# Optimization experiments

Hardware: AMD Instinct MI355X
Metric: run time of the kernel (lower is better)

## Reference

```python
import jax, jax.numpy as jnp
import numpy as np

N = 50000      # nodes
E = 800000     # edges (avg degree 16)
D = 128        # feature / channel width (channel_counts=[128,128,128])
HEAD = 64      # head_dim
NEG_SLOPE = 0.2  # PyG GATConv leaky_relu slope


def setup_inputs() -> dict:
    key = jax.random.key(0)
    ks = jax.random.split(key, 32)
    s = 1.0 / np.sqrt(D)

    def w(k, shape):
        return jax.random.normal(k, shape, jnp.float32) * s

    return {
        "x": jax.random.normal(ks[0], (N, D), jnp.float32),
        "edge_index": jax.random.randint(ks[1], (2, E), 0, N, dtype=jnp.int32),
        # layer 0: lazy (-1,-1) GATConv -> separate src/dst linear maps
        "w0_src": w(ks[2], (D, D)), "w0_dst": w(ks[3], (D, D)),
        "a0_src": w(ks[4], (D,)), "a0_dst": w(ks[5], (D,)),
        "bc0": jnp.zeros((D,), jnp.float32),
        "wl0": w(ks[6], (D, D)), "bl0": jnp.zeros((D,), jnp.float32),
        # layer 1: int in_channels -> shared weight
        "w1": w(ks[7], (D, D)),
        "a1_src": w(ks[8], (D,)), "a1_dst": w(ks[9], (D,)),
        "bc1": jnp.zeros((D,), jnp.float32),
        "wl1": w(ks[10], (D, D)), "bl1": jnp.zeros((D,), jnp.float32),
        # layer 2
        "w2": w(ks[11], (D, D)),
        "a2_src": w(ks[12], (D,)), "a2_dst": w(ks[13], (D,)),
        "bc2": jnp.zeros((D,), jnp.float32),
        "wl2": w(ks[14], (D, D)), "bl2": jnp.zeros((D,), jnp.float32),
        # head linear
        "wh": w(ks[15], (D, HEAD)), "bh": jnp.zeros((HEAD,), jnp.float32),
    }


def _gat(h_src, h_dst, src, dst, a_src, a_dst, bias):
    """PyG GATConv (heads=1, no self loops, eval-mode). h_*: [N,C]."""
    al_s = h_src @ a_src                                   # [N]
    al_d = h_dst @ a_dst                                   # [N]
    logits = jax.nn.leaky_relu(al_s[src] + al_d[dst], NEG_SLOPE)  # [E]
    m = jax.ops.segment_max(logits, dst, num_segments=N)  # per-dest max
    e = jnp.exp(logits - m[dst])
    denom = jax.ops.segment_sum(e, dst, num_segments=N)
    alpha = e / denom[dst]                                 # [E]
    msg = h_src[src] * alpha[:, None]                      # [E,C]
    return jax.ops.segment_sum(msg, dst, num_segments=N) + bias


def reference(x, edge_index, w0_src, w0_dst, a0_src, a0_dst, bc0, wl0, bl0,
              w1, a1_src, a1_dst, bc1, wl1, bl1,
              w2, a2_src, a2_dst, bc2, wl2, bl2, wh, bh):
    src, dst = edge_index[0], edge_index[1]
    # layer 0: conv(x) + lin(x), relu
    h = _gat(x @ w0_src, x @ w0_dst, src, dst, a0_src, a0_dst, bc0) + x @ wl0 + bl0
    h = jax.nn.relu(h)
    # layer 1: shared-weight conv
    hs = h @ w1
    h = _gat(hs, hs, src, dst, a1_src, a1_dst, bc1) + h @ wl1 + bl1
    h = jax.nn.relu(h)
    # layer 2 (no relu)
    hs = h @ w2
    h = _gat(hs, hs, src, dst, a2_src, a2_dst, bc2) + h @ wl2 + bl2
    # head
    return h @ wh + bh
```

## Files before the change

kernel.cpp:

```cpp
#include <hip/hip_runtime.h>

#define NNODE 50000
#define NEDGE 800000
#define DIM   128
#define NEG   0.2f
#define NBUCK 196
#define EPB1  2048
#define NB1   391
#define GBLK  782
#define GN    12500
#define SB_PA (NB1)
#define SB_PH (SB_PA + 32)
#define SB_MV (SB_PH + 9)
#define SB_CV (SB_MV + 193)
#define SB_TOT (SB_CV + GN)

typedef __attribute__((ext_vector_type(8))) short bf16x8;
typedef __attribute__((ext_vector_type(4))) float f32x4;

__device__ __forceinline__ float wmax(float v){
  #pragma unroll
  for (int m = 32; m > 0; m >>= 1) v = fmaxf(v, __shfl_xor(v, m));
  return v;
}
__device__ __forceinline__ float wsum(float v){
  #pragma unroll
  for (int m = 32; m > 0; m >>= 1) v += __shfl_xor(v, m);
  return v;
}
__device__ __forceinline__ unsigned short f2bf(float f){
  unsigned int x = __float_as_uint(f);
  return (unsigned short)((x + 0x7fffu + ((x >> 16) & 1u)) >> 16);
}
__device__ __forceinline__ float bflo(unsigned u){ return __uint_as_float(u << 16); }
__device__ __forceinline__ float bfhi(unsigned u){ return __uint_as_float(u & 0xffff0000u); }

__global__ __launch_bounds__(256) void setup_k(
    const int* __restrict__ ei,
    const float* __restrict__ x,
    const float* __restrict__ w0s, const float* __restrict__ a0s,
    const float* __restrict__ w0d, const float* __restrict__ a0d,
    const float* __restrict__ bc0, const float* __restrict__ wl0,
    const float* __restrict__ bl0,
    const float* __restrict__ w1,  const float* __restrict__ a1s,
    const float* __restrict__ a1d, const float* __restrict__ bc1,
    const float* __restrict__ wl1, const float* __restrict__ bl1,
    const float* __restrict__ w2,  const float* __restrict__ a2s,
    const float* __restrict__ a2d, const float* __restrict__ bc2,
    const float* __restrict__ wl2, const float* __restrict__ bl2,
    const float* __restrict__ wh,  const float* __restrict__ bh,
    int* __restrict__ cnt,
    unsigned short* __restrict__ Wz1, unsigned short* __restrict__ Wz2,
    unsigned short* __restrict__ Wz3, float* __restrict__ bf3,
    float* __restrict__ uv, float* __restrict__ bf1, float* __restrict__ bf2,
    unsigned int* __restrict__ Xb, float* __restrict__ als, float* __restrict__ ald){
  int bid = blockIdx.x;

  if (bid < NB1){
    __shared__ int h[NBUCK];
    const int* dst = ei + NEDGE;
    for (int i = threadIdx.x; i < NBUCK; i += 256) h[i] = 0;
    __syncthreads();
    int e0 = bid * EPB1 + threadIdx.x;
    #pragma unroll
    for (int i = 0; i < 8; ++i){
      int e = e0 + i * 256;
      if (e < NEDGE) atomicAdd(&h[dst[e] >> 8], 1);
    }
    __syncthreads();
    for (int i = threadIdx.x; i < NBUCK; i += 256)
      cnt[i * NB1 + bid] = h[i];
    return;
  }
  if (bid < SB_PH){
    int g = (bid - SB_PA) * 256 + threadIdx.x;
    int layer = g >> 12;
    int rem = g & 4095;
    int ct = rem >> 9, q = (rem >> 6) & 7, lane = rem & 63;
    int quad = lane >> 4;
    int c = ct * 16 + (lane & 15);
    const float* wA = layer ? w1 : w0s;
    const float* wB = layer ? wl1 : wl0;
    unsigned short* dst = (layer ? Wz2 : Wz1) + ((size_t)(ct * 8 + q) * 64 + lane) * 8;
    #pragma unroll
    for (int j = 0; j < 8; ++j){
      int k = q * 32 + quad * 8 + j;
      float v = (k < 128) ? wA[k * 128 + c] : wB[(k - 128) * 128 + c];
      dst[j] = f2bf(v);
    }
    return;
  }
  if (bid < SB_MV){
    int pb = bid - SB_PH;
    if (pb == 8){
      int c = threadIdx.x;
      if (c < 64){
        float s = bh[c];
        for (int t = 0; t < 128; ++t) s += (bc2[t] + bl2[t]) * wh[t * 64 + c];
        bf3[c] = s;
      }
      return;
    }
    int g = pb * 256 + threadIdx.x;
    int ct = g >> 9, q = (g >> 6) & 7, lane = g & 63;
    int quad = lane >> 4;
    int c = ct * 16 + (lane & 15);
    unsigned short* dst = Wz3 + ((size_t)(ct * 8 + q) * 64 + lane) * 8;
    #pragma unroll
    for (int j = 0; j < 8; ++j){
      int k = q * 32 + quad * 8 + j;
      const float* src = (k < 128) ? (w2 + k * 128) : (wl2 + (k - 128) * 128);
      float s = 0.f;
      for (int t = 0; t < 128; ++t) s += src[t] * wh[t * 64 + c];
      dst[j] = f2bf(s);
    }
    return;
  }
  if (bid < SB_CV){
    int mb = bid - SB_MV;
    if (mb == 192){
      int t = threadIdx.x;
      if (t < 128) bf1[t] = bc0[t] + bl0[t];
      else bf2[t - 128] = bc1[t - 128] + bl1[t - 128];
      return;
    }
    int lane = threadIdx.x & 63;
    int idx = mb * 4 + (threadIdx.x >> 6);
    int grp = idx >> 7, r = idx & 127;
    const float* W; const float* a;
    switch (grp){
      case 0: W = w0s; a = a0s; break;
      case 1: W = w0d; a = a0d; break;
      case 2: W = w1;  a = a1s; break;
      case 3: W = w1;  a = a1d; break;
      case 4: W = w2;  a = a2s; break;
      default: W = w2; a = a2d; break;
    }
    float2 w = ((const float2*)(W + r * DIM))[lane];
    float2 av = ((const float2*)a)[lane];
    float s = wsum(w.x * av.x + w.y * av.y);
    if (lane == 0) uv[grp * 128 + r] = s;
    return;
  }
  {
    int lane = threadIdx.x & 63;
    int n = (bid - SB_CV) * 4 + (threadIdx.x >> 6);
    if (n >= NNODE) return;
    float2 xv = ((const float2*)(x + (size_t)n * DIM))[lane];
    Xb[(size_t)n * 64 + lane] = (unsigned)f2bf(xv.x) | ((unsigned)f2bf(xv.y) << 16);
    float2 uu = ((const float2*)uv)[lane];
    float2 vv = ((const float2*)(uv + 128))[lane];
    float s1 = wsum(xv.x * uu.x + xv.y * uu.y);
    float s2 = wsum(xv.x * vv.x + xv.y * vv.y);
    if (lane == 0){ als[n] = s1; ald[n] = s2; }
  }
}


__global__ __launch_bounds__(256) void dual_k(const float* __restrict__ X,
                                              const float* __restrict__ uv,
                                              float* __restrict__ als,
                                              float* __restrict__ ald){
  int lane = threadIdx.x & 63;
  int n = blockIdx.x * 4 + (threadIdx.x >> 6);
  if (n >= NNODE) return;
  float2 xv = ((const float2*)(X + (size_t)n * DIM))[lane];
  float2 uu = ((const float2*)uv)[lane];
  float2 vv = ((const float2*)(uv + 128))[lane];
  float s1 = wsum(xv.x * uu.x + xv.y * uu.y);
  float s2 = wsum(xv.x * vv.x + xv.y * vv.y);
  if (lane == 0){ als[n] = s1; ald[n] = s2; }
}

__global__ __launch_bounds__(256) void scan196_k(const int* __restrict__ cnt,
                                                 int* __restrict__ cbase,
                                                 int* __restrict__ btot){
  __shared__ int sd[256];
  int b = blockIdx.x, t = threadIdx.x;
  const int* row = cnt + (size_t)b * NB1;
  int i0 = t * 2, i1 = t * 2 + 1;
  int v0 = (i0 < NB1) ? row[i0] : 0;
  int v1 = (i1 < NB1) ? row[i1] : 0;
  int s = v0 + v1;
  sd[t] = s; __syncthreads();
  #pragma unroll
  for (int off = 1; off < 256; off <<= 1){
    int u = (t >= off) ? sd[t - off] : 0;
    __syncthreads();
    sd[t] += u;
    __syncthreads();
  }
  int ex = sd[t] - s;
  if (i0 < NB1) cbase[(size_t)b * NB1 + i0] = ex;
  if (i1 < NB1) cbase[(size_t)b * NB1 + i1] = ex + v0;
  if (t == 255) btot[b] = sd[255];
}

__global__ __launch_bounds__(256) void bscan2_k(const int* __restrict__ btot,
                                                int* __restrict__ gbase,
                                                int* __restrict__ rp){
  __shared__ int sd[256];
  int t = threadIdx.x;
  int v = (t < NBUCK) ? btot[t] : 0;
  sd[t] = v; __syncthreads();
  #pragma unroll
  for (int off = 1; off < 256; off <<= 1){
    int u = (t >= off) ? sd[t - off] : 0;
    __syncthreads();
    sd[t] += u;
    __syncthreads();
  }
  if (t < NBUCK) gbase[t] = sd[t] - v;
  if (t == NBUCK - 1) gbase[NBUCK] = sd[t];
  if (t == 0) rp[NNODE] = NEDGE;
}

__global__ __launch_bounds__(256) void scat2_k(const int* __restrict__ ei,
                                               const int* __restrict__ gbase,
                                               const int* __restrict__ cbase,
                                               unsigned int* __restrict__ packed){
  __shared__ int lcur[NBUCK];
  for (int i = threadIdx.x; i < NBUCK; i += 256) lcur[i] = 0;
  __syncthreads();
  int e0 = blockIdx.x * EPB1 + threadIdx.x;
  #pragma unroll
  for (int i = 0; i < 8; ++i){
    int e = e0 + i * 256;
    if (e < NEDGE){
      int s = ei[e], d = ei[NEDGE + e];
      int b = d >> 8;
      int r = atomicAdd(&lcur[b], 1);
      int pos = gbase[b] + cbase[(size_t)b * NB1 + blockIdx.x] + r;
      packed[pos] = ((unsigned)d << 16) | (unsigned)s;
    }
  }
}

__global__ __launch_bounds__(256) void build_k(const int* __restrict__ gbase,
                                               const unsigned int* __restrict__ packed,
                                               int* __restrict__ rp,
                                               unsigned short* __restrict__ es){
  __shared__ int h[256], sd[256], cur[256];
  int b = blockIdx.x, t = threadIdx.x;
  int s0 = gbase[b], s1 = gbase[b + 1];
  h[t] = 0; __syncthreads();
  for (int i = s0 + t; i < s1; i += 256)
    atomicAdd(&h[(packed[i] >> 16) & 255], 1);
  __syncthreads();
  int v = h[t]; sd[t] = v; __syncthreads();
  #pragma unroll
  for (int off = 1; off < 256; off <<= 1){
    int u = (t >= off) ? sd[t - off] : 0;
    __syncthreads();
    sd[t] += u;
    __syncthreads();
  }
  int ex = sd[t] - v;
  cur[t] = ex;
  int d = b * 256 + t;
  if (d < NNODE) rp[d] = s0 + ex;
  __syncthreads();
  for (int i = s0 + t; i < s1; i += 256){
    unsigned int p = packed[i];
    int ld = (p >> 16) & 255;
    int pos = atomicAdd(&cur[ld], 1);
    es[s0 + pos] = (unsigned short)(p & 0xffffu);
  }
}

__global__ __launch_bounds__(256) void gat_k(const int* __restrict__ rp,
                                             const unsigned short* __restrict__ es,
                                             const float* __restrict__ als,
                                             const float* __restrict__ ald,
                                             const unsigned int* __restrict__ A,
                                             unsigned int* __restrict__ Mb){
  int lane = threadIdx.x & 63;
  int n = blockIdx.x * 4 + (threadIdx.x >> 6);
  if (n >= NNODE) return;
  int start = rp[n], end = rp[n + 1];
  int deg = end - start;
  float ad = ald[n];
  float2 acc = make_float2(0.f, 0.f);
  float rinv = 0.f;

  if (deg <= 64){
    int s = 0; float z = -3.0e38f;
    if (lane < deg){
      s = es[start + lane];
      float t = als[s] + ad;
      z = t > 0.f ? t : NEG * t;
    }
    float m = wmax(z);
    float e = (lane < deg) ? __expf(z - m) : 0.f;
    float denom = wsum(e);
    rinv = (deg > 0) ? 1.f / denom : 0.f;
    int dq = (deg + 7) & ~7;
    for (int j = 0; j < dq; j += 8){
      int   s0 = __shfl(s, j),     s1 = __shfl(s, j + 1);
      int   s2 = __shfl(s, j + 2), s3 = __shfl(s, j + 3);
      int   s4 = __shfl(s, j + 4), s5 = __shfl(s, j + 5);
      int   s6 = __shfl(s, j + 6), s7 = __shfl(s, j + 7);
      float w0 = __shfl(e, j),     w1 = __shfl(e, j + 1);
      float w2 = __shfl(e, j + 2), w3 = __shfl(e, j + 3);
      float w4 = __shfl(e, j + 4), w5 = __shfl(e, j + 5);
      float w6 = __shfl(e, j + 6), w7 = __shfl(e, j + 7);
      unsigned p0 = A[(size_t)s0 * 64 + lane];
      unsigned p1 = A[(size_t)s1 * 64 + lane];
      unsigned p2 = A[(size_t)s2 * 64 + lane];
      unsigned p3 = A[(size_t)s3 * 64 + lane];
      unsigned p4 = A[(size_t)s4 * 64 + lane];
      unsigned p5 = A[(size_t)s5 * 64 + lane];
      unsigned p6 = A[(size_t)s6 * 64 + lane];
      unsigned p7 = A[(size_t)s7 * 64 + lane];
      acc.x = fmaf(w0, bflo(p0), acc.x); acc.y = fmaf(w0, bfhi(p0), acc.y);
      acc.x = fmaf(w1, bflo(p1), acc.x); acc.y = fmaf(w1, bfhi(p1), acc.y);
      acc.x = fmaf(w2, bflo(p2), acc.x); acc.y = fmaf(w2, bfhi(p2), acc.y);
      acc.x = fmaf(w3, bflo(p3), acc.x); acc.y = fmaf(w3, bfhi(p3), acc.y);
      acc.x = fmaf(w4, bflo(p4), acc.x); acc.y = fmaf(w4, bfhi(p4), acc.y);
      acc.x = fmaf(w5, bflo(p5), acc.x); acc.y = fmaf(w5, bfhi(p5), acc.y);
      acc.x = fmaf(w6, bflo(p6), acc.x); acc.y = fmaf(w6, bfhi(p6), acc.y);
      acc.x = fmaf(w7, bflo(p7), acc.x); acc.y = fmaf(w7, bfhi(p7), acc.y);
    }
  } else {
    float mloc = -3.0e38f;
    for (int i = start + lane; i < end; i += 64){
      int s = es[i];
      float zz = als[s] + ad;
      zz = zz > 0.f ? zz : NEG * zz;
      mloc = fmaxf(mloc, zz);
    }
    float m = wmax(mloc);
    float dloc = 0.f;
    for (int i = start + lane; i < end; i += 64){
      int s = es[i];
      float zz = als[s] + ad;
      zz = zz > 0.f ? zz : NEG * zz;
      dloc += __expf(zz - m);
    }
    rinv = 1.f / wsum(dloc);
    for (int i = start; i < end; ++i){
      int s = es[i];
      float zz = als[s] + ad;
      zz = zz > 0.f ? zz : NEG * zz;
      float w = __expf(zz - m);
      unsigned p = A[(size_t)s * 64 + lane];
      acc.x = fmaf(w, bflo(p), acc.x);
      acc.y = fmaf(w, bfhi(p), acc.y);
    }
  }

  Mb[(size_t)n * 64 + lane] =
      (unsigned)f2bf(acc.x * rinv) | ((unsigned)f2bf(acc.y * rinv) << 16);
}

template<int FINAL>
__global__ __launch_bounds__(256) void mfma_k(const unsigned int* __restrict__ Mb,
                                              const unsigned int* __restrict__ Hin,
                                              const unsigned short* __restrict__ Wz,
                                              const float* __restrict__ bias,
                                              const float* __restrict__ u,
                                              const float* __restrict__ v,
                                              unsigned short* __restrict__ Hout,
                                              float* __restrict__ outf,
                                              float* __restrict__ als,
                                              float* __restrict__ ald){
  int lane = threadIdx.x & 63;
  int wid  = threadIdx.x >> 6;
  int r0   = blockIdx.x * 64 + wid * 16;
  int quad = lane >> 4;
  int col  = lane & 15;

  int rA = r0 + col; if (rA > NNODE - 1) rA = NNODE - 1;
  const bf16x8* mrow = (const bf16x8*)(Mb + (size_t)rA * 64);
  const bf16x8* hrow = (const bf16x8*)(Hin + (size_t)rA * 64);
  bf16x8 a[8];
  #pragma unroll
  for (int q = 0; q < 4; ++q){
    a[q]     = mrow[q * 4 + quad];
    a[q + 4] = hrow[q * 4 + quad];
  }

  const bf16x8* wz = (const bf16x8*)Wz;
  int rowq = r0 + quad * 4;
  float alsp[4] = {0.f, 0.f, 0.f, 0.f};
  float aldp[4] = {0.f, 0.f, 0.f, 0.f};
  const int NCT = FINAL ? 4 : 8;

  #pragma unroll
  for (int ct = 0; ct < NCT; ++ct){
    f32x4 acc = {0.f, 0.f, 0.f, 0.f};
    #pragma unroll
    for (int q = 0; q < 8; ++q){
      bf16x8 bfr = wz[(ct * 8 + q) * 64 + lane];
      acc = __builtin_amdgcn_mfma_f32_16x16x32_bf16(a[q], bfr, acc, 0, 0, 0);
    }
    int c = ct * 16 + col;
    float bb = bias[c];
    if (FINAL){
      #pragma unroll
      for (int r = 0; r < 4; ++r){
        int row = rowq + r;
        if (row < NNODE) outf[(size_t)row * 64 + c] = acc[r] + bb;
      }
    } else {
      float uc = u[c], vc = v[c];
      #pragma unroll
      for (int r = 0; r < 4; ++r){
        float h = fmaxf(acc[r] + bb, 0.f);
        alsp[r] = fmaf(h, uc, alsp[r]);
        aldp[r] = fmaf(h, vc, aldp[r]);
        int row = rowq + r;
        if (row < NNODE) Hout[(size_t)row * 128 + c] = f2bf(h);
      }
    }
  }

  if (!FINAL){
    #pragma unroll
    for (int m = 1; m < 16; m <<= 1){
      #pragma unroll
      for (int r = 0; r < 4; ++r){
        alsp[r] += __shfl_xor(alsp[r], m);
        aldp[r] += __shfl_xor(aldp[r], m);
      }
    }
    if (col == 0){
      #pragma unroll
      for (int r = 0; r < 4; ++r){
        int row = rowq + r;
        if (row < NNODE){ als[row] = alsp[r]; ald[row] = aldp[r]; }
      }
    }
  }
}

extern "C" void kernel_launch(void* const* d_in, const int* in_sizes, int n_in,
                              void* d_out, int out_size, void* d_ws, size_t ws_size,
                              hipStream_t stream){
  const float* x   = (const float*)d_in[0];
  const int*   ei  = (const int*)d_in[1];
  const float* w0s = (const float*)d_in[2];
  const float* w0d = (const float*)d_in[3];
  const float* a0s = (const float*)d_in[4];
  const float* a0d = (const float*)d_in[5];
  const float* bc0 = (const float*)d_in[6];
  const float* wl0 = (const float*)d_in[7];
  const float* bl0 = (const float*)d_in[8];
  const float* w1  = (const float*)d_in[9];
  const float* a1s = (const float*)d_in[10];
  const float* a1d = (const float*)d_in[11];
  const float* bc1 = (const float*)d_in[12];
  const float* wl1 = (const float*)d_in[13];
  const float* bl1 = (const float*)d_in[14];
  const float* w2  = (const float*)d_in[15];
  const float* a2s = (const float*)d_in[16];
  const float* a2d = (const float*)d_in[17];
  const float* bc2 = (const float*)d_in[18];
  const float* wl2 = (const float*)d_in[19];
  const float* bl2 = (const float*)d_in[20];
  const float* wh  = (const float*)d_in[21];
  const float* bh  = (const float*)d_in[22];
  float* out = (float*)d_out;

  unsigned int* Xb = (unsigned int*)d_ws;
  unsigned int* Ha = Xb + (size_t)NNODE * 64;
  unsigned int* Hb = Ha + (size_t)NNODE * 64;
  unsigned int* Mb = Hb + (size_t)NNODE * 64;
  float* alsA = (float*)(Mb + (size_t)NNODE * 64);
  float* aldA = alsA + NNODE;
  float* alsB = aldA + NNODE;
  float* aldB = alsB + NNODE;
  float* uv   = aldB + NNODE;
  float* bf1  = uv + 6 * 128;
  float* bf2  = bf1 + 128;
  float* bf3  = bf2 + 128;
  unsigned short* Wz1 = (unsigned short*)(bf3 + 64);
  unsigned short* Wz2 = Wz1 + 256 * 128;
  unsigned short* Wz3 = Wz2 + 256 * 128;
  int*   rp    = (int*)(Wz3 + 256 * 64);
  int*   cnt   = rp + (NNODE + 1);
  int*   cbase = cnt + NBUCK * NB1;
  int*   btot  = cbase + NBUCK * NB1;
  int*   gbase = btot + NBUCK;
  unsigned int* packed = (unsigned int*)(gbase + (NBUCK + 1));
  unsigned short* es   = (unsigned short*)(packed + NEDGE);

  dim3 b(256);
  dim3 gn(GN);

  setup_k<<<SB_TOT, b, 0, stream>>>(ei, x,
      w0s, a0s, w0d, a0d, bc0, wl0, bl0,
      w1, a1s, a1d, bc1, wl1, bl1,
      w2, a2s, a2d, bc2, wl2, bl2, wh, bh,
      cnt, Wz1, Wz2, Wz3, bf3, uv, bf1, bf2, Xb, alsA, aldA);

  dual_k<<<gn, b, 0, stream>>>(x, uv, alsA, aldA);

  scan196_k<<<NBUCK, b, 0, stream>>>(cnt, cbase, btot);
  bscan2_k<<<1, b, 0, stream>>>(btot, gbase, rp);
  scat2_k<<<NB1, b, 0, stream>>>(ei, gbase, cbase, packed);
  build_k<<<NBUCK, b, 0, stream>>>(gbase, packed, rp, es);

  gat_k<<<gn, b, 0, stream>>>(rp, es, alsA, aldA, Xb, Mb);
  mfma_k<0><<<GBLK, b, 0, stream>>>(Mb, Xb, Wz1, bf1, uv + 2 * 128, uv + 3 * 128,
                                    (unsigned short*)Ha, nullptr, alsB, aldB);

  gat_k<<<gn, b, 0, stream>>>(rp, es, alsB, aldB, Ha, Mb);
  mfma_k<0><<<GBLK, b, 0, stream>>>(Mb, Ha, Wz2, bf2, uv + 4 * 128, uv + 5 * 128,
                                    (unsigned short*)Hb, nullptr, alsA, aldA);

  gat_k<<<gn, b, 0, stream>>>(rp, es, alsA, aldA, Hb, Mb);
  mfma_k<1><<<GBLK, b, 0, stream>>>(Mb, Hb, Wz3, bf3, nullptr, nullptr,
                                    nullptr, out, nullptr, nullptr);
}
```

Measured before the change: 314.7 us.

## Vectorize GAT neighbor gather with uint4 loads and fold dual kernel into scan

```diff
diff --git a/kernel.cpp b/kernel.cpp
--- a/kernel.cpp
+++ b/kernel.cpp
@@ -53,7 +53,7 @@
     unsigned short* __restrict__ Wz1, unsigned short* __restrict__ Wz2,
     unsigned short* __restrict__ Wz3, float* __restrict__ bf3,
     float* __restrict__ uv, float* __restrict__ bf1, float* __restrict__ bf2,
-    unsigned int* __restrict__ Xb, float* __restrict__ als, float* __restrict__ ald){
+    unsigned int* __restrict__ Xb){
   int bid = blockIdx.x;
 
   if (bid < NB1){
@@ -148,28 +148,7 @@
     if (n >= NNODE) return;
     float2 xv = ((const float2*)(x + (size_t)n * DIM))[lane];
     Xb[(size_t)n * 64 + lane] = (unsigned)f2bf(xv.x) | ((unsigned)f2bf(xv.y) << 16);
-    float2 uu = ((const float2*)uv)[lane];
-    float2 vv = ((const float2*)(uv + 128))[lane];
-    float s1 = wsum(xv.x * uu.x + xv.y * uu.y);
-    float s2 = wsum(xv.x * vv.x + xv.y * vv.y);
-    if (lane == 0){ als[n] = s1; ald[n] = s2; }
-  }
-}
-
-
-__global__ __launch_bounds__(256) void dual_k(const float* __restrict__ X,
-                                              const float* __restrict__ uv,
-                                              float* __restrict__ als,
-                                              float* __restrict__ ald){
-  int lane = threadIdx.x & 63;
-  int n = blockIdx.x * 4 + (threadIdx.x >> 6);
-  if (n >= NNODE) return;
-  float2 xv = ((const float2*)(X + (size_t)n * DIM))[lane];
-  float2 uu = ((const float2*)uv)[lane];
-  float2 vv = ((const float2*)(uv + 128))[lane];
-  float s1 = wsum(xv.x * uu.x + xv.y * uu.y);
-  float s2 = wsum(xv.x * vv.x + xv.y * vv.y);
-  if (lane == 0){ als[n] = s1; ald[n] = s2; }
+  }
 }
 
 __global__ __launch_bounds__(256) void scan196_k(const int* __restrict__ cnt,
@@ -198,7 +177,23 @@
 
 __global__ __launch_bounds__(256) void bscan2_k(const int* __restrict__ btot,
                                                 int* __restrict__ gbase,
-                                                int* __restrict__ rp){
+                                                int* __restrict__ rp,
+                                                const float* __restrict__ X,
+                                                const float* __restrict__ uv,
+                                                float* __restrict__ als,
+                                                float* __restrict__ ald){
+  if (blockIdx.x > 0){
+    int lane = threadIdx.x & 63;
+    int n = (blockIdx.x - 1) * 4 + (threadIdx.x >> 6);
+    if (n >= NNODE) return;
+    float2 xv = ((const float2*)(X + (size_t)n * DIM))[lane];
+    float2 uu = ((const float2*)uv)[lane];
+    float2 vv = ((const float2*)(uv + 128))[lane];
+    float s1 = wsum(xv.x * uu.x + xv.y * uu.y);
+    float s2 = wsum(xv.x * vv.x + xv.y * vv.y);
+    if (lane == 0){ als[n] = s1; ald[n] = s2; }
+    return;
+  }
   __shared__ int sd[256];
   int t = threadIdx.x;
   int v = (t < NBUCK) ? btot[t] : 0;
@@ -280,8 +275,6 @@
   int start = rp[n], end = rp[n + 1];
   int deg = end - start;
   float ad = ald[n];
-  float2 acc = make_float2(0.f, 0.f);
-  float rinv = 0.f;
 
   if (deg <= 64){
     int s = 0; float z = -3.0e38f;
@@ -293,35 +286,43 @@
     float m = wmax(z);
     float e = (lane < deg) ? __expf(z - m) : 0.f;
     float denom = wsum(e);
-    rinv = (deg > 0) ? 1.f / denom : 0.f;
+    float rinv = (deg > 0) ? 1.f / denom : 0.f;
+
+    int half = lane >> 4;
+    int sub  = lane & 15;
+    const uint4* A4 = (const uint4*)A;
+    float a0 = 0.f, a1 = 0.f, a2 = 0.f, a3 = 0.f;
+    float a4 = 0.f, a5 = 0.f, a6 = 0.f, a7 = 0.f;
     int dq = (deg + 7) & ~7;
     for (int j = 0; j < dq; j += 8){
-      int   s0 = __shfl(s, j),     s1 = __shfl(s, j + 1);
-      int   s2 = __shfl(s, j + 2), s3 = __shfl(s, j + 3);
-      int   s4 = __shfl(s, j + 4), s5 = __shfl(s, j + 5);
-      int   s6 = __shfl(s, j + 6), s7 = __shfl(s, j + 7);
-      float w0 = __shfl(e, j),     w1 = __shfl(e, j + 1);
-      float w2 = __shfl(e, j + 2), w3 = __shfl(e, j + 3);
-      float w4 = __shfl(e, j + 4), w5 = __shfl(e, j + 5);
-      float w6 = __shfl(e, j + 6), w7 = __shfl(e, j + 7);
-      unsigned p0 = A[(size_t)s0 * 64 + lane];
-      unsigned p1 = A[(size_t)s1 * 64 + lane];
-      unsigned p2 = A[(size_t)s2 * 64 + lane];
-      unsigned p3 = A[(size_t)s3 * 64 + lane];
-      unsigned p4 = A[(size_t)s4 * 64 + lane];
-      unsigned p5 = A[(size_t)s5 * 64 + lane];
-      unsigned p6 = A[(size_t)s6 * 64 + lane];
-      unsigned p7 = A[(size_t)s7 * 64 + lane];
-      acc.x = fmaf(w0, bflo(p0), acc.x); acc.y = fmaf(w0, bfhi(p0), acc.y);
-      acc.x = fmaf(w1, bflo(p1), acc.x); acc.y = fmaf(w1, bfhi(p1), acc.y);
-      acc.x = fmaf(w2, bflo(p2), acc.x); acc.y = fmaf(w2, bfhi(p2), acc.y);
-      acc.x = fmaf(w3, bflo(p3), acc.x); acc.y = fmaf(w3, bfhi(p3), acc.y);
-      acc.x = fmaf(w4, bflo(p4), acc.x); acc.y = fmaf(w4, bfhi(p4), acc.y);
-      acc.x = fmaf(w5, bflo(p5), acc.x); acc.y = fmaf(w5, bfhi(p5), acc.y);
-      acc.x = fmaf(w6, bflo(p6), acc.x); acc.y = fmaf(w6, bfhi(p6), acc.y);
-      acc.x = fmaf(w7, bflo(p7), acc.x); acc.y = fmaf(w7, bfhi(p7), acc.y);
+      int   sA = __shfl(s, j + half);
+      int   sB = __shfl(s, j + 4 + half);
+      float wA = __shfl(e, j + half);
+      float wB = __shfl(e, j + 4 + half);
+      uint4 pA = A4[(size_t)sA * 16 + sub];
+      uint4 pB = A4[(size_t)sB * 16 + sub];
+      a0 = fmaf(wA, bflo(pA.x), a0); a1 = fmaf(wA, bfhi(pA.x), a1);
+      a2 = fmaf(wA, bflo(pA.y), a2); a3 = fmaf(wA, bfhi(pA.y), a3);
+      a4 = fmaf(wA, bflo(pA.z), a4); a5 = fmaf(wA, bfhi(pA.z), a5);
+      a6 = fmaf(wA, bflo(pA.w), a6); a7 = fmaf(wA, bfhi(pA.w), a7);
+      a0 = fmaf(wB, bflo(pB.x), a0); a1 = fmaf(wB, bfhi(pB.x), a1);
+      a2 = fmaf(wB, bflo(pB.y), a2); a3 = fmaf(wB, bfhi(pB.y), a3);
+      a4 = fmaf(wB, bflo(pB.z), a4); a5 = fmaf(wB, bfhi(pB.z), a5);
+      a6 = fmaf(wB, bflo(pB.w), a6); a7 = fmaf(wB, bfhi(pB.w), a7);
+    }
+    #define RED(v) v += __shfl_xor(v, 16); v += __shfl_xor(v, 32);
+    RED(a0) RED(a1) RED(a2) RED(a3) RED(a4) RED(a5) RED(a6) RED(a7)
+    #undef RED
+    if (half == 0){
+      uint4 o;
+      o.x = (unsigned)f2bf(a0 * rinv) | ((unsigned)f2bf(a1 * rinv) << 16);
+      o.y = (unsigned)f2bf(a2 * rinv) | ((unsigned)f2bf(a3 * rinv) << 16);
+      o.z = (unsigned)f2bf(a4 * rinv) | ((unsigned)f2bf(a5 * rinv) << 16);
+      o.w = (unsigned)f2bf(a6 * rinv) | ((unsigned)f2bf(a7 * rinv) << 16);
+      ((uint4*)(Mb + (size_t)n * 64))[sub] = o;
     }
   } else {
+    float2 acc = make_float2(0.f, 0.f);
     float mloc = -3.0e38f;
     for (int i = start + lane; i < end; i += 64){
       int s = es[i];
@@ -337,7 +338,7 @@
       zz = zz > 0.f ? zz : NEG * zz;
       dloc += __expf(zz - m);
     }
-    rinv = 1.f / wsum(dloc);
+    float rinv = 1.f / wsum(dloc);
     for (int i = start; i < end; ++i){
       int s = es[i];
       float zz = als[s] + ad;
@@ -347,10 +348,9 @@
       acc.x = fmaf(w, bflo(p), acc.x);
       acc.y = fmaf(w, bfhi(p), acc.y);
     }
-  }
-
-  Mb[(size_t)n * 64 + lane] =
-      (unsigned)f2bf(acc.x * rinv) | ((unsigned)f2bf(acc.y * rinv) << 16);
+    Mb[(size_t)n * 64 + lane] =
+        (unsigned)f2bf(acc.x * rinv) | ((unsigned)f2bf(acc.y * rinv) << 16);
+  }
 }
 
 template<int FINAL>
@@ -492,12 +492,10 @@
       w0s, a0s, w0d, a0d, bc0, wl0, bl0,
       w1, a1s, a1d, bc1, wl1, bl1,
       w2, a2s, a2d, bc2, wl2, bl2, wh, bh,
-      cnt, Wz1, Wz2, Wz3, bf3, uv, bf1, bf2, Xb, alsA, aldA);
-
-  dual_k<<<gn, b, 0, stream>>>(x, uv, alsA, aldA);
+      cnt, Wz1, Wz2, Wz3, bf3, uv, bf1, bf2, Xb);
 
   scan196_k<<<NBUCK, b, 0, stream>>>(cnt, cbase, btot);
-  bscan2_k<<<1, b, 0, stream>>>(btot, gbase, rp);
+  bscan2_k<<<1 + GN, b, 0, stream>>>(btot, gbase, rp, x, uv, alsA, aldA);
   scat2_k<<<NB1, b, 0, stream>>>(ei, gbase, cbase, packed);
   build_k<<<NBUCK, b, 0, stream>>>(gbase, packed, rp, es);
 
```

After: 307.0 us. -2.4%, faster.
